# Kernel tuning notes

Hardware: AMD Instinct MI355X
Metric: run time of the kernel (lower is better)

The kernel has to match this reference:

```python
import jax, jax.numpy as jnp
from jax import lax
import numpy as np

B, T, D, H, LAT, FUT = 2048, 64, 64, 256, 64, 96
NL = 10  # LSTM layers


def _lstm_layer(x, Wih, Whh, b):
    # x: [B, T, Din]; Wih: [4H, Din]; Whh: [4H, H]; b: [4H]
    xg = jnp.einsum('btd,gd->tbg', x, Wih) + b  # precompute input projections [T,B,4H]
    h0 = jnp.zeros((x.shape[0], Whh.shape[1]), x.dtype)

    def step(carry, xt):
        h, c = carry
        g = xt + h @ Whh.T
        i, f, gg, o = jnp.split(g, 4, axis=-1)  # torch gate order i,f,g,o
        c = jax.nn.sigmoid(f) * c + jax.nn.sigmoid(i) * jnp.tanh(gg)
        h = jax.nn.sigmoid(o) * jnp.tanh(c)
        return (h, c), h

    _, hs = lax.scan(step, (h0, h0), xg)
    return jnp.transpose(hs, (1, 0, 2))  # [B,T,H]


def setup_inputs() -> dict:
    key = jax.random.key(0)
    ks = iter(jax.random.split(key, 40))
    s = 0.05
    n = lambda shape: jax.random.normal(next(ks), shape, jnp.float32) * s
    inp = {
        'X': jax.random.normal(next(ks), (B, T, D), jnp.float32),
        'Wih0': n((4 * H, D)),
        'Wih': n((NL - 1, 4 * H, H)),
        'Whh': n((NL, 4 * H, H)),
        'b': n((NL, 4 * H)),  # b_ih + b_hh folded together
        'ef1w': n((128, H)), 'ef1b': n((128,)),
        'ef2w': n((64, 128)), 'ef2b': n((64,)),
        'mean_w': n((LAT, 64)), 'mean_b': n((LAT,)),
        'logvar_w': n((LAT, 64)), 'logvar_b': n((LAT,)),
        'scale_w': n((LAT, 64)), 'scale_b': n((LAT,)),
        'shape_w': n((LAT, 64)), 'shape_b': n((LAT,)),
        'df1w': n((128, LAT)), 'df1b': n((128,)),
        'df2w': n((500, 128)), 'df2b': n((500,)),
        'outw': n((FUT, 500)), 'outb': n((FUT,)),
        'finw': n((FUT, FUT)), 'finb': n((FUT,)),
        'pi_gaussian': jnp.asarray(0.9, jnp.float32),
        'eps': jax.random.normal(next(ks), (B, LAT), jnp.float32),
        'u': jax.random.uniform(next(ks), (B, LAT), jnp.float32),
        'choice': jax.random.uniform(next(ks), (B,), jnp.float32),
    }
    return inp


def reference(X, Wih0, Wih, Whh, b, ef1w, ef1b, ef2w, ef2b,
              mean_w, mean_b, logvar_w, logvar_b, scale_w, scale_b,
              shape_w, shape_b, df1w, df1b, df2w, df2b, outw, outb,
              finw, finb, pi_gaussian, eps, u, choice):
    # ---- Encoder: 10-layer LSTM, last hidden state ----
    h = _lstm_layer(X, Wih0, Whh[0], b[0])
    for l in range(1, NL):
        h = _lstm_layer(h, Wih[l - 1], Whh[l], b[l])
    last = h[:, -1, :]  # [B,H]
    hid = jax.nn.relu(last @ ef1w.T + ef1b)
    hid = jax.nn.relu(hid @ ef2w.T + ef2b)  # dropout = identity (eval)
    z_mean = hid @ mean_w.T + mean_b
    z_logvar = hid @ logvar_w.T + logvar_b
    z_scale = jnp.exp(hid @ scale_w.T + scale_b)
    z_shape = hid @ shape_w.T + shape_b
    # ---- Reparameterize: vectorized gaussian/GPD row selection ----
    z_gauss = z_mean + eps * jnp.exp(0.5 * z_logvar)
    z_gpd = z_scale / z_shape * (jnp.exp(-z_shape * jnp.log1p(-u)) - 1.0)
    z = jnp.where(choice[:, None] < pi_gaussian, z_gauss, z_gpd)
    # ---- Decoder ----
    d = jax.nn.relu(z @ df1w.T + df1b)
    d = jax.nn.relu(d @ df2w.T + df2b)
    out = d @ outw.T + outb
    final = out @ finw.T + finb
    return (final, z_mean, z_logvar, z_scale, z_shape)
```

## Files before the change

### kernel.cpp

```cpp
#include <hip/hip_runtime.h>

typedef unsigned short u16;
typedef unsigned int   u32;
typedef _Float16 v8hf __attribute__((ext_vector_type(8)));
typedef float  f32x4 __attribute__((ext_vector_type(4)));

static constexpr int B_   = 2048;
static constexpr int T_   = 64;
static constexpr int D_   = 64;
static constexpr int H_   = 256;
static constexpr int NL_  = 10;
static constexpr int FUT_ = 96;
static constexpr int NBLK = 128;

static constexpr size_t WFH_OFF  = 0;
static constexpr size_t WFX_OFF  = 5u << 20;
static constexpr size_t XG_OFF   = 10u << 20;
static constexpr size_t SEQ2_OFF = 26u << 20;
static constexpr int    WFL9 = 262144;
static constexpr int    TCH  = 4;

__device__ __forceinline__ u16 f2h(float f) {
  _Float16 h = (_Float16)f;
  return __builtin_bit_cast(u16, h);
}
__device__ __forceinline__ float h2f(u16 b) {
  return (float)__builtin_bit_cast(_Float16, b);
}
__device__ __forceinline__ float rcp_(float x) { return __builtin_amdgcn_rcpf(x); }
__device__ __forceinline__ float fsig(float x) { return rcp_(1.f + __expf(-x)); }
__device__ __forceinline__ float ftanh(float x) {
  float e = __expf(-2.f * fabsf(x));
  float t = (1.f - e) * rcp_(1.f + e);
  return copysignf(t, x);
}
__device__ __forceinline__ void gld16(const u16* g, u16* l) {
  __builtin_amdgcn_global_load_lds(
      (const __attribute__((address_space(1))) void*)g,
      (__attribute__((address_space(3))) void*)l,
      16, 0, 0);
}

__global__ void pack_weights_v13(const float* __restrict__ Wih0,
                                 const float* __restrict__ Wih,
                                 const float* __restrict__ Whh,
                                 u16* __restrict__ wfh,
                                 u16* __restrict__ wfx) {
  int gid = blockIdx.x * 256 + threadIdx.x;
  int lw  = gid >> 15;
  if (lw >= NL_ * 2) return;
  int l = lw >> 1, which = lw & 1;
  int rem  = gid & 32767;
  int kc   = rem >> 12;
  int cg   = (rem >> 8) & 15;
  int g    = (rem >> 6) & 3;
  int lane = rem & 63;
  if (which == 1 && l == 0 && kc >= 2) return;

  int row = g * 256 + cg * 16 + (lane & 15);
  int k0  = kc * 32 + (lane >> 4) * 8;

  float v[8];
#pragma unroll
  for (int i = 0; i < 8; ++i) {
    int k = k0 + i;
    float x;
    if (which == 0)      x = Whh[(size_t)(l * 1024 + row) * 256 + k];
    else if (l == 0)     x = Wih0[row * 64 + k];
    else                 x = Wih[(size_t)((l - 1) * 1024 + row) * 256 + k];
    v[i] = x;
  }
  u32 pk[4];
#pragma unroll
  for (int i = 0; i < 4; ++i)
    pk[i] = (u32)f2h(v[2 * i]) | ((u32)f2h(v[2 * i + 1]) << 16);
  uint4 val; val.x = pk[0]; val.y = pk[1]; val.z = pk[2]; val.w = pk[3];
  u16* base = (which == 0) ? wfh : wfx;
  u16* dst = base + (size_t)l * WFL9
                  + ((size_t)(kc * 16 + cg) * 4 + g) * 512 + (size_t)lane * 8;
  *(uint4*)dst = val;
}

template <bool L0>
__global__ __launch_bounds__(1024, 4) void lstm_layer_v13(
    const float* __restrict__ X,
    u16* __restrict__ seq,
    const u16* __restrict__ wfx_l,
    const u16* __restrict__ wfh_l,
    u16* __restrict__ xg,
    const float* __restrict__ bias) {
  __shared__ __align__(16) u16 Wring[65536];
  __shared__ __align__(16) u16 Ah[16 * 256];

  const int tid  = threadIdx.x;
  const int wid  = tid >> 6;
  const int lane = tid & 63;
  const int bid  = blockIdx.x;
  const int arow = lane & 15;
  const int ahi  = lane >> 4;
  const int j    = wid * 16 + arow;

  *(uint2*)((char*)Ah + tid * 8) = make_uint2(0, 0);

  float c[4] = {0.f, 0.f, 0.f, 0.f};
  float bv[4];
#pragma unroll
  for (int g = 0; g < 4; ++g) bv[g] = bias[g * 256 + j];

  u16* slot0 = Wring + wid * 2048;
  u16* slot1 = Wring + 32768 + wid * 2048;
  const size_t laneoff = (size_t)lane * 8;
  u16* xgb = xg + (size_t)bid * 65536;
  uint2 xr[4];

  v8hf whr[4][4];
#pragma unroll
  for (int kc = 0; kc < 4; ++kc)
#pragma unroll
    for (int g = 0; g < 4; ++g)
      whr[kc][g] = *(const v8hf*)(const void*)(
          wfh_l + ((size_t)(kc * 16 + wid) * 4 + g) * 512 + laneoff);

  __syncthreads();

  for (int tc = 0; tc < T_ / TCH; ++tc) {
    f32x4 acc0[TCH][4];
#pragma unroll
    for (int rf = 0; rf < TCH; ++rf)
#pragma unroll
      for (int g = 0; g < 4; ++g) {
        acc0[rf][g][0] = bv[g]; acc0[rf][g][1] = bv[g];
        acc0[rf][g][2] = bv[g]; acc0[rf][g][3] = bv[g];
      }

    if constexpr (L0) {
#pragma unroll
      for (int g = 0; g < 4; ++g) {
        gld16(wfx_l + ((size_t)(0 * 16 + wid) * 4 + g) * 512 + laneoff, slot0 + g * 512);
        gld16(wfx_l + ((size_t)(1 * 16 + wid) * 4 + g) * 512 + laneoff, slot1 + g * 512);
      }
      asm volatile("s_waitcnt vmcnt(0)" ::: "memory");
      __builtin_amdgcn_sched_barrier(0);
      const float* xb = X + ((size_t)(bid * 16 + arow) * T_ + tc * TCH) * D_ + ahi * 8;
#pragma unroll
      for (int kc = 0; kc < 2; ++kc) {
        const u16* wl = (kc ? slot1 : slot0) + lane * 8;
        v8hf af[TCH];
#pragma unroll
        for (int rf = 0; rf < TCH; ++rf) {
          float4 u = *(const float4*)(xb + rf * D_ + kc * 32);
          float4 v2 = *(const float4*)(xb + rf * D_ + kc * 32 + 4);
          v8hf a;
          a[0] = (_Float16)u.x;  a[1] = (_Float16)u.y;
          a[2] = (_Float16)u.z;  a[3] = (_Float16)u.w;
          a[4] = (_Float16)v2.x; a[5] = (_Float16)v2.y;
          a[6] = (_Float16)v2.z; a[7] = (_Float16)v2.w;
          af[rf] = a;
        }
#pragma unroll
        for (int g = 0; g < 4; ++g) {
          v8hf w = *(const v8hf*)(const void*)(wl + g * 512);
#pragma unroll
          for (int rf = 0; rf < TCH; ++rf)
            acc0[rf][g] = __builtin_amdgcn_mfma_f32_16x16x32_f16(af[rf], w, acc0[rf][g], 0, 0, 0);
        }
      }
    } else {
      const u16* abase = seq + ((size_t)(bid * T_ + tc * TCH) * 16 + arow) * 256 + ahi * 8;
      v8hf aA[TCH], aB[TCH];
#pragma unroll
      for (int g = 0; g < 4; ++g)
        gld16(wfx_l + ((size_t)(0 * 16 + wid) * 4 + g) * 512 + laneoff, slot0 + g * 512);
#pragma unroll
      for (int rf = 0; rf < TCH; ++rf)
        aA[rf] = *(const v8hf*)(const void*)(abase + rf * 4096);

#pragma unroll
      for (int kc = 0; kc < 8; ++kc) {
        if (kc < 7) {
          u16* nd = ((kc + 1) & 1) ? slot1 : slot0;
#pragma unroll
          for (int g = 0; g < 4; ++g)
            gld16(wfx_l + ((size_t)((kc + 1) * 16 + wid) * 4 + g) * 512 + laneoff, nd + g * 512);
          if ((kc & 1) == 0) {
#pragma unroll
            for (int rf = 0; rf < TCH; ++rf)
              aB[rf] = *(const v8hf*)(const void*)(abase + rf * 4096 + (kc + 1) * 32);
          } else {
#pragma unroll
            for (int rf = 0; rf < TCH; ++rf)
              aA[rf] = *(const v8hf*)(const void*)(abase + rf * 4096 + (kc + 1) * 32);
          }
          asm volatile("s_waitcnt vmcnt(8)" ::: "memory");
        } else {
          asm volatile("s_waitcnt vmcnt(0)" ::: "memory");
        }
        __builtin_amdgcn_sched_barrier(0);
        const u16* wl = ((kc & 1) ? slot1 : slot0) + lane * 8;
#pragma unroll
        for (int g = 0; g < 4; ++g) {
          v8hf w = *(const v8hf*)(const void*)(wl + g * 512);
#pragma unroll
          for (int rf = 0; rf < TCH; ++rf)
            acc0[rf][g] = __builtin_amdgcn_mfma_f32_16x16x32_f16(
                ((kc & 1) ? aB[rf] : aA[rf]), w, acc0[rf][g], 0, 0, 0);
        }
      }
    }

#pragma unroll
    for (int rf = 0; rf < TCH; ++rf)
#pragma unroll
      for (int g = 0; g < 4; ++g) {
        uint2 pk;
        pk.x = (u32)f2h(acc0[rf][g][0]) | ((u32)f2h(acc0[rf][g][1]) << 16);
        pk.y = (u32)f2h(acc0[rf][g][2]) | ((u32)f2h(acc0[rf][g][3]) << 16);
        *(uint2*)(xgb + (((size_t)(rf * 1024 + g * 256 + j)) << 4) + ahi * 4) = pk;
      }
    __syncthreads();

#pragma unroll
    for (int g = 0; g < 4; ++g)
      xr[g] = *(const uint2*)(xgb + (((size_t)(0 * 1024 + g * 256 + j)) << 4) + ahi * 4);

    for (int tl = 0; tl < TCH; ++tl) {
      const int t = tc * TCH + tl;
      f32x4 acc[4];
#pragma unroll
      for (int g = 0; g < 4; ++g) {
        acc[g][0] = h2f((u16)(xr[g].x & 0xffff));
        acc[g][1] = h2f((u16)(xr[g].x >> 16));
        acc[g][2] = h2f((u16)(xr[g].y & 0xffff));
        acc[g][3] = h2f((u16)(xr[g].y >> 16));
      }

#pragma unroll
      for (int g = 0; g < 4; ++g)
        gld16(wfh_l + ((size_t)(4 * 16 + wid) * 4 + g) * 512 + laneoff, slot0 + g * 512);
#pragma unroll
      for (int g = 0; g < 4; ++g)
        gld16(wfh_l + ((size_t)(5 * 16 + wid) * 4 + g) * 512 + laneoff, slot1 + g * 512);

#pragma unroll
      for (int kc = 0; kc < 4; ++kc) {
        v8hf a = *(const v8hf*)((const char*)Ah + arow * 512 +
                                ((kc * 64 + ahi * 16) ^ ((arow & 7) << 4)));
#pragma unroll
        for (int g = 0; g < 4; ++g)
          acc[g] = __builtin_amdgcn_mfma_f32_16x16x32_f16(a, whr[kc][g], acc[g], 0, 0, 0);
      }

      asm volatile("s_waitcnt vmcnt(4)" ::: "memory");
      __builtin_amdgcn_sched_barrier(0);
      {
        v8hf a = *(const v8hf*)((const char*)Ah + arow * 512 +
                                ((4 * 64 + ahi * 16) ^ ((arow & 7) << 4)));
        const u16* wl = slot0 + lane * 8;
#pragma unroll
        for (int g = 0; g < 4; ++g) {
          v8hf w = *(const v8hf*)(const void*)(wl + g * 512);
          acc[g] = __builtin_amdgcn_mfma_f32_16x16x32_f16(a, w, acc[g], 0, 0, 0);
        }
      }
#pragma unroll
      for (int g = 0; g < 4; ++g)
        gld16(wfh_l + ((size_t)(6 * 16 + wid) * 4 + g) * 512 + laneoff, slot0 + g * 512);
      asm volatile("s_waitcnt vmcnt(4)" ::: "memory");
      __builtin_amdgcn_sched_barrier(0);
      {
        v8hf a = *(const v8hf*)((const char*)Ah + arow * 512 +
                                ((5 * 64 + ahi * 16) ^ ((arow & 7) << 4)));
        const u16* wl = slot1 + lane * 8;
#pragma unroll
        for (int g = 0; g < 4; ++g) {
          v8hf w = *(const v8hf*)(const void*)(wl + g * 512);
          acc[g] = __builtin_amdgcn_mfma_f32_16x16x32_f16(a, w, acc[g], 0, 0, 0);
        }
      }
#pragma unroll
      for (int g = 0; g < 4; ++g)
        gld16(wfh_l + ((size_t)(7 * 16 + wid) * 4 + g) * 512 + laneoff, slot1 + g * 512);
      asm volatile("s_waitcnt vmcnt(4)" ::: "memory");
      __builtin_amdgcn_sched_barrier(0);
      {
        v8hf a = *(const v8hf*)((const char*)Ah + arow * 512 +
                                ((6 * 64 + ahi * 16) ^ ((arow & 7) << 4)));
        const u16* wl = slot0 + lane * 8;
#pragma unroll
        for (int g = 0; g < 4; ++g) {
          v8hf w = *(const v8hf*)(const void*)(wl + g * 512);
          acc[g] = __builtin_amdgcn_mfma_f32_16x16x32_f16(a, w, acc[g], 0, 0, 0);
        }
      }
      asm volatile("s_waitcnt vmcnt(0)" ::: "memory");
      __builtin_amdgcn_sched_barrier(0);
      {
        v8hf a = *(const v8hf*)((const char*)Ah + arow * 512 +
                                ((7 * 64 + ahi * 16) ^ ((arow & 7) << 4)));
        const u16* wl = slot1 + lane * 8;
#pragma unroll
        for (int g = 0; g < 4; ++g) {
          v8hf w = *(const v8hf*)(const void*)(wl + g * 512);
          acc[g] = __builtin_amdgcn_mfma_f32_16x16x32_f16(a, w, acc[g], 0, 0, 0);
        }
      }
      __syncthreads();

      if (tl + 1 < TCH) {
#pragma unroll
        for (int g = 0; g < 4; ++g)
          xr[g] = *(const uint2*)(xgb + (((size_t)((tl + 1) * 1024 + g * 256 + j)) << 4) + ahi * 4);
      }

      u16* sbase = seq + ((((size_t)bid * T_ + t) * 16) << 8) + j;
#pragma unroll
      for (int q = 0; q < 4; ++q) {
        int r = ahi * 4 + q;
        float cn = fsig(acc[1][q]) * c[q] + fsig(acc[0][q]) * ftanh(acc[2][q]);
        c[q] = cn;
        float h = fsig(acc[3][q]) * ftanh(cn);
        u16 hb = f2h(h);
        sbase[(size_t)r << 8] = hb;
        *(u16*)((char*)Ah + r * 512 + ((j * 2) ^ ((r & 7) << 4))) = hb;
      }
      __syncthreads();
    }
  }
}

template <int N, int K, bool RELU>
__device__ __forceinline__ void dense(const float (*__restrict__ in)[512],
                                      float (*__restrict__ out)[512],
                                      const float* __restrict__ W,
                                      const float* __restrict__ bg, int tid) {
  for (int e = tid; e < 16 * N; e += 256) {
    int r = e / N, n = e - r * N;
    const float* wr = W + (size_t)n * K;
    const float* ar = in[r];
    float4 acc = {0.f, 0.f, 0.f, 0.f};
    for (int k = 0; k < K; k += 4) {
      float4 wv = *(const float4*)(wr + k);
      float4 av = *(const float4*)(ar + k);
      acc.x = fmaf(wv.x, av.x, acc.x);
      acc.y = fmaf(wv.y, av.y, acc.y);
      acc.z = fmaf(wv.z, av.z, acc.z);
      acc.w = fmaf(wv.w, av.w, acc.w);
    }
    float s = bg[n] + acc.x + acc.y + acc.z + acc.w;
    out[r][n] = RELU ? fmaxf(s, 0.f) : s;
  }
}

template <int K>
__device__ __forceinline__ float dotK(const float* __restrict__ a, const float* __restrict__ w) {
  float4 acc = {0.f, 0.f, 0.f, 0.f};
#pragma unroll
  for (int k = 0; k < K; k += 4) {
    float4 wv = *(const float4*)(w + k);
    float4 av = *(const float4*)(a + k);
    acc.x = fmaf(wv.x, av.x, acc.x);
    acc.y = fmaf(wv.y, av.y, acc.y);
    acc.z = fmaf(wv.z, av.z, acc.z);
    acc.w = fmaf(wv.w, av.w, acc.w);
  }
  return acc.x + acc.y + acc.z + acc.w;
}

struct TailArgs {
  const u16* seq;
  const float *ef1w, *ef1b, *ef2w, *ef2b;
  const float *mean_w, *mean_b, *logvar_w, *logvar_b;
  const float *scale_w, *scale_b, *shape_w, *shape_b;
  const float *df1w, *df1b, *df2w, *df2b, *outw, *outb, *finw, *finb;
  const float *pi, *eps, *u, *choice;
  float* out;
};

__global__ __launch_bounds__(256) void tail_kernel_v13(TailArgs A) {
  __shared__ float a0[16][512];
  __shared__ float a1[16][512];
  const int tid = threadIdx.x, bid = blockIdx.x;

  for (int e = tid; e < 16 * 256; e += 256) {
    int r = e >> 8, jj = e & 255;
    a0[r][jj] = h2f(A.seq[((((size_t)bid * T_ + (T_ - 1)) * 16 + r) << 8) + jj]);
  }
  __syncthreads();

  dense<128, 256, true>(a0, a1, A.ef1w, A.ef1b, tid); __syncthreads();
  dense<64, 128, true>(a1, a0, A.ef2w, A.ef2b, tid);  __syncthreads();

  const float pi = *A.pi;
  for (int e = tid; e < 16 * 64; e += 256) {
    int r = e >> 6, n = e & 63;
    size_t rg = (size_t)bid * 16 + r;
    float m  = dotK<64>(a0[r], A.mean_w   + n * 64) + A.mean_b[n];
    float lv = dotK<64>(a0[r], A.logvar_w + n * 64) + A.logvar_b[n];
    float sc = __expf(dotK<64>(a0[r], A.scale_w + n * 64) + A.scale_b[n]);
    float sh = dotK<64>(a0[r], A.shape_w + n * 64) + A.shape_b[n];
    A.out[196608 + rg * 64 + n] = m;
    A.out[327680 + rg * 64 + n] = lv;
    A.out[458752 + rg * 64 + n] = sc;
    A.out[589824 + rg * 64 + n] = sh;
    float zg = m + A.eps[rg * 64 + n] * __expf(0.5f * lv);
    float L  = log1pf(-A.u[rg * 64 + n]);
    float zp = sc / sh * (__expf(-sh * L) - 1.f);
    a1[r][n] = (A.choice[rg] < pi) ? zg : zp;
  }
  __syncthreads();

  dense<128, 64, true>(a1, a0, A.df1w, A.df1b, tid);   __syncthreads();
  dense<500, 128, true>(a0, a1, A.df2w, A.df2b, tid);  __syncthreads();
  dense<96, 500, false>(a1, a0, A.outw, A.outb, tid);  __syncthreads();
  dense<96, 96, false>(a0, a1, A.finw, A.finb, tid);   __syncthreads();

  for (int e = tid; e < 16 * FUT_; e += 256) {
    int r = e / FUT_, n = e - r * FUT_;
    A.out[((size_t)bid * 16 + r) * FUT_ + n] = a1[r][n];
  }
}

extern "C" void kernel_launch(void* const* d_in, const int* in_sizes, int n_in,
                              void* d_out, int out_size, void* d_ws, size_t ws_size,
                              hipStream_t stream) {
  (void)in_sizes; (void)n_in; (void)out_size; (void)ws_size;

  const float* X      = (const float*)d_in[0];
  const float* Wih0   = (const float*)d_in[1];
  const float* Wih    = (const float*)d_in[2];
  const float* Whh    = (const float*)d_in[3];
  const float* b      = (const float*)d_in[4];
  const float* ef1w   = (const float*)d_in[5];
  const float* ef1b   = (const float*)d_in[6];
  const float* ef2w   = (const float*)d_in[7];
  const float* ef2b   = (const float*)d_in[8];
  const float* mean_w = (const float*)d_in[9];
  const float* mean_b = (const float*)d_in[10];
  const float* logvar_w = (const float*)d_in[11];
  const float* logvar_b = (const float*)d_in[12];
  const float* scale_w  = (const float*)d_in[13];
  const float* scale_b  = (const float*)d_in[14];
  const float* shape_w  = (const float*)d_in[15];
  const float* shape_b  = (const float*)d_in[16];
  const float* df1w   = (const float*)d_in[17];
  const float* df1b   = (const float*)d_in[18];
  const float* df2w   = (const float*)d_in[19];
  const float* df2b   = (const float*)d_in[20];
  const float* outw   = (const float*)d_in[21];
  const float* outb   = (const float*)d_in[22];
  const float* finw   = (const float*)d_in[23];
  const float* finb   = (const float*)d_in[24];
  const float* pi_g   = (const float*)d_in[25];
  const float* eps    = (const float*)d_in[26];
  const float* u      = (const float*)d_in[27];
  const float* choice = (const float*)d_in[28];

  float* out = (float*)d_out;
  u16* wfh = (u16*)((char*)d_ws + WFH_OFF);
  u16* wfx = (u16*)((char*)d_ws + WFX_OFF);
  u16* xg  = (u16*)((char*)d_ws + XG_OFF);
  u16* seq = (u16*)((char*)d_ws + SEQ2_OFF);

  pack_weights_v13<<<2560, 256, 0, stream>>>(Wih0, Wih, Whh, wfh, wfx);

  lstm_layer_v13<true><<<NBLK, 1024, 0, stream>>>(X, seq, wfx, wfh, xg, b);
  for (int l = 1; l < NL_; ++l)
    lstm_layer_v13<false><<<NBLK, 1024, 0, stream>>>(nullptr, seq,
        wfx + (size_t)l * WFL9, wfh + (size_t)l * WFL9, xg, b + l * 1024);

  TailArgs A;
  A.seq = seq;
  A.ef1w = ef1w; A.ef1b = ef1b; A.ef2w = ef2w; A.ef2b = ef2b;
  A.mean_w = mean_w; A.mean_b = mean_b; A.logvar_w = logvar_w; A.logvar_b = logvar_b;
  A.scale_w = scale_w; A.scale_b = scale_b; A.shape_w = shape_w; A.shape_b = shape_b;
  A.df1w = df1w; A.df1b = df1b; A.df2w = df2w; A.df2b = df2b;
  A.outw = outw; A.outb = outb; A.finw = finw; A.finb = finb;
  A.pi = pi_g; A.eps = eps; A.u = u; A.choice = choice;
  A.out = out;
  tail_kernel_v13<<<NBLK, 256, 0, stream>>>(A);
}
```

Before: 11.93 ms.

## Keep input-gate projections in registers and stream all recurrent weights through LDS

The input projections for each time chunk are now packed to fp16 and kept in registers (xr[TCH][4]). Before, they were written to a global xg scratch buffer and read back. This removes the global round trip and a block-wide barrier. The recurrent weight chunks 0-3 that used to live in registers (whr) are now streamed through the LDS double-buffer ring like chunks 4-7, with an 8-step pipelined loop. That frees registers but adds global-to-LDS weight traffic every time step, which raises load latency on the serial recurrence path.

Measured after the change: 11.09 ms. 1.08x faster.

```diff
diff --git a/kernel.cpp b/kernel.cpp
--- a/kernel.cpp
+++ b/kernel.cpp
@@ -15,7 +15,6 @@
 
 static constexpr size_t WFH_OFF  = 0;
 static constexpr size_t WFX_OFF  = 5u << 20;
-static constexpr size_t XG_OFF   = 10u << 20;
 static constexpr size_t SEQ2_OFF = 26u << 20;
 static constexpr int    WFL9 = 262144;
 static constexpr int    TCH  = 4;
@@ -41,7 +40,7 @@
       16, 0, 0);
 }
 
-__global__ void pack_weights_v13(const float* __restrict__ Wih0,
+__global__ void pack_weights_v14(const float* __restrict__ Wih0,
                                  const float* __restrict__ Wih,
                                  const float* __restrict__ Whh,
                                  u16* __restrict__ wfh,
@@ -82,12 +81,11 @@
 }
 
 template <bool L0>
-__global__ __launch_bounds__(1024, 4) void lstm_layer_v13(
+__global__ __launch_bounds__(1024, 4) void lstm_layer_v14(
     const float* __restrict__ X,
     u16* __restrict__ seq,
     const u16* __restrict__ wfx_l,
     const u16* __restrict__ wfh_l,
-    u16* __restrict__ xg,
     const float* __restrict__ bias) {
   __shared__ __align__(16) u16 Wring[65536];
   __shared__ __align__(16) u16 Ah[16 * 256];
@@ -110,16 +108,6 @@
   u16* slot0 = Wring + wid * 2048;
   u16* slot1 = Wring + 32768 + wid * 2048;
   const size_t laneoff = (size_t)lane * 8;
-  u16* xgb = xg + (size_t)bid * 65536;
-  uint2 xr[4];
-
-  v8hf whr[4][4];
-#pragma unroll
-  for (int kc = 0; kc < 4; ++kc)
-#pragma unroll
-    for (int g = 0; g < 4; ++g)
-      whr[kc][g] = *(const v8hf*)(const void*)(
-          wfh_l + ((size_t)(kc * 16 + wid) * 4 + g) * 512 + laneoff);
 
   __syncthreads();
 
@@ -209,99 +197,53 @@
     }
 
 #pragma unroll
+    for (int g = 0; g < 4; ++g)
+      gld16(wfh_l + ((size_t)(0 * 16 + wid) * 4 + g) * 512 + laneoff, slot0 + g * 512);
+#pragma unroll
+    for (int g = 0; g < 4; ++g)
+      gld16(wfh_l + ((size_t)(1 * 16 + wid) * 4 + g) * 512 + laneoff, slot1 + g * 512);
+
+    uint2 xr[TCH][4];
+#pragma unroll
     for (int rf = 0; rf < TCH; ++rf)
 #pragma unroll
       for (int g = 0; g < 4; ++g) {
-        uint2 pk;
-        pk.x = (u32)f2h(acc0[rf][g][0]) | ((u32)f2h(acc0[rf][g][1]) << 16);
-        pk.y = (u32)f2h(acc0[rf][g][2]) | ((u32)f2h(acc0[rf][g][3]) << 16);
-        *(uint2*)(xgb + (((size_t)(rf * 1024 + g * 256 + j)) << 4) + ahi * 4) = pk;
-      }
-    __syncthreads();
-
-#pragma unroll
-    for (int g = 0; g < 4; ++g)
-      xr[g] = *(const uint2*)(xgb + (((size_t)(0 * 1024 + g * 256 + j)) << 4) + ahi * 4);
-
+        xr[rf][g].x = (u32)f2h(acc0[rf][g][0]) | ((u32)f2h(acc0[rf][g][1]) << 16);
+        xr[rf][g].y = (u32)f2h(acc0[rf][g][2]) | ((u32)f2h(acc0[rf][g][3]) << 16);
+      }
+
+#pragma unroll
     for (int tl = 0; tl < TCH; ++tl) {
       const int t = tc * TCH + tl;
       f32x4 acc[4];
 #pragma unroll
       for (int g = 0; g < 4; ++g) {
-        acc[g][0] = h2f((u16)(xr[g].x & 0xffff));
-        acc[g][1] = h2f((u16)(xr[g].x >> 16));
-        acc[g][2] = h2f((u16)(xr[g].y & 0xffff));
-        acc[g][3] = h2f((u16)(xr[g].y >> 16));
-      }
-
-#pragma unroll
-      for (int g = 0; g < 4; ++g)
-        gld16(wfh_l + ((size_t)(4 * 16 + wid) * 4 + g) * 512 + laneoff, slot0 + g * 512);
-#pragma unroll
-      for (int g = 0; g < 4; ++g)
-        gld16(wfh_l + ((size_t)(5 * 16 + wid) * 4 + g) * 512 + laneoff, slot1 + g * 512);
-
-#pragma unroll
-      for (int kc = 0; kc < 4; ++kc) {
+        acc[g][0] = h2f((u16)(xr[tl][g].x & 0xffff));
+        acc[g][1] = h2f((u16)(xr[tl][g].x >> 16));
+        acc[g][2] = h2f((u16)(xr[tl][g].y & 0xffff));
+        acc[g][3] = h2f((u16)(xr[tl][g].y >> 16));
+      }
+
+#pragma unroll
+      for (int kc = 0; kc < 8; ++kc) {
+        if (kc < 7) asm volatile("s_waitcnt vmcnt(4)" ::: "memory");
+        else        asm volatile("s_waitcnt vmcnt(0)" ::: "memory");
+        __builtin_amdgcn_sched_barrier(0);
+
         v8hf a = *(const v8hf*)((const char*)Ah + arow * 512 +
                                 ((kc * 64 + ahi * 16) ^ ((arow & 7) << 4)));
-#pragma unroll
-        for (int g = 0; g < 4; ++g)
-          acc[g] = __builtin_amdgcn_mfma_f32_16x16x32_f16(a, whr[kc][g], acc[g], 0, 0, 0);
-      }
-
-      asm volatile("s_waitcnt vmcnt(4)" ::: "memory");
-      __builtin_amdgcn_sched_barrier(0);
-      {
-        v8hf a = *(const v8hf*)((const char*)Ah + arow * 512 +
-                                ((4 * 64 + ahi * 16) ^ ((arow & 7) << 4)));
-        const u16* wl = slot0 + lane * 8;
+        const u16* wl = ((kc & 1) ? slot1 : slot0) + lane * 8;
 #pragma unroll
         for (int g = 0; g < 4; ++g) {
           v8hf w = *(const v8hf*)(const void*)(wl + g * 512);
           acc[g] = __builtin_amdgcn_mfma_f32_16x16x32_f16(a, w, acc[g], 0, 0, 0);
         }
-      }
-#pragma unroll
-      for (int g = 0; g < 4; ++g)
-        gld16(wfh_l + ((size_t)(6 * 16 + wid) * 4 + g) * 512 + laneoff, slot0 + g * 512);
-      asm volatile("s_waitcnt vmcnt(4)" ::: "memory");
-      __builtin_amdgcn_sched_barrier(0);
-      {
-        v8hf a = *(const v8hf*)((const char*)Ah + arow * 512 +
-                                ((5 * 64 + ahi * 16) ^ ((arow & 7) << 4)));
-        const u16* wl = slot1 + lane * 8;
-#pragma unroll
-        for (int g = 0; g < 4; ++g) {
-          v8hf w = *(const v8hf*)(const void*)(wl + g * 512);
-          acc[g] = __builtin_amdgcn_mfma_f32_16x16x32_f16(a, w, acc[g], 0, 0, 0);
-        }
-      }
-#pragma unroll
-      for (int g = 0; g < 4; ++g)
-        gld16(wfh_l + ((size_t)(7 * 16 + wid) * 4 + g) * 512 + laneoff, slot1 + g * 512);
-      asm volatile("s_waitcnt vmcnt(4)" ::: "memory");
-      __builtin_amdgcn_sched_barrier(0);
-      {
-        v8hf a = *(const v8hf*)((const char*)Ah + arow * 512 +
-                                ((6 * 64 + ahi * 16) ^ ((arow & 7) << 4)));
-        const u16* wl = slot0 + lane * 8;
-#pragma unroll
-        for (int g = 0; g < 4; ++g) {
-          v8hf w = *(const v8hf*)(const void*)(wl + g * 512);
-          acc[g] = __builtin_amdgcn_mfma_f32_16x16x32_f16(a, w, acc[g], 0, 0, 0);
-        }
-      }
-      asm volatile("s_waitcnt vmcnt(0)" ::: "memory");
-      __builtin_amdgcn_sched_barrier(0);
-      {
-        v8hf a = *(const v8hf*)((const char*)Ah + arow * 512 +
-                                ((7 * 64 + ahi * 16) ^ ((arow & 7) << 4)));
-        const u16* wl = slot1 + lane * 8;
-#pragma unroll
-        for (int g = 0; g < 4; ++g) {
-          v8hf w = *(const v8hf*)(const void*)(wl + g * 512);
-          acc[g] = __builtin_amdgcn_mfma_f32_16x16x32_f16(a, w, acc[g], 0, 0, 0);
+        if (kc < 6) {
+          u16* nd = (kc & 1) ? slot1 : slot0;
+#pragma unroll
+          for (int g = 0; g < 4; ++g)
+            gld16(wfh_l + ((size_t)((kc + 2) * 16 + wid) * 4 + g) * 512 + laneoff,
+                  nd + g * 512);
         }
       }
       __syncthreads();
@@ -309,7 +251,10 @@
       if (tl + 1 < TCH) {
 #pragma unroll
         for (int g = 0; g < 4; ++g)
-          xr[g] = *(const uint2*)(xgb + (((size_t)((tl + 1) * 1024 + g * 256 + j)) << 4) + ahi * 4);
+          gld16(wfh_l + ((size_t)(0 * 16 + wid) * 4 + g) * 512 + laneoff, slot0 + g * 512);
+#pragma unroll
+        for (int g = 0; g < 4; ++g)
+          gld16(wfh_l + ((size_t)(1 * 16 + wid) * 4 + g) * 512 + laneoff, slot1 + g * 512);
       }
 
       u16* sbase = seq + ((((size_t)bid * T_ + t) * 16) << 8) + j;
@@ -376,7 +321,7 @@
   float* out;
 };
 
-__global__ __launch_bounds__(256) void tail_kernel_v13(TailArgs A) {
+__global__ __launch_bounds__(256) void tail_kernel_v14(TailArgs A) {
   __shared__ float a0[16][512];
   __shared__ float a1[16][512];
   const int tid = threadIdx.x, bid = blockIdx.x;
@@ -458,15 +403,14 @@
   float* out = (float*)d_out;
   u16* wfh = (u16*)((char*)d_ws + WFH_OFF);
   u16* wfx = (u16*)((char*)d_ws + WFX_OFF);
-  u16* xg  = (u16*)((char*)d_ws + XG_OFF);
   u16* seq = (u16*)((char*)d_ws + SEQ2_OFF);
 
-  pack_weights_v13<<<2560, 256, 0, stream>>>(Wih0, Wih, Whh, wfh, wfx);
-
-  lstm_layer_v13<true><<<NBLK, 1024, 0, stream>>>(X, seq, wfx, wfh, xg, b);
+  pack_weights_v14<<<2560, 256, 0, stream>>>(Wih0, Wih, Whh, wfh, wfx);
+
+  lstm_layer_v14<true><<<NBLK, 1024, 0, stream>>>(X, seq, wfx, wfh, b);
   for (int l = 1; l < NL_; ++l)
-    lstm_layer_v13<false><<<NBLK, 1024, 0, stream>>>(nullptr, seq,
-        wfx + (size_t)l * WFL9, wfh + (size_t)l * WFL9, xg, b + l * 1024);
+    lstm_layer_v14<false><<<NBLK, 1024, 0, stream>>>(nullptr, seq,
+        wfx + (size_t)l * WFL9, wfh + (size_t)l * WFL9, b + l * 1024);
 
   TailArgs A;
   A.seq = seq;
@@ -477,5 +421,5 @@
   A.outw = outw; A.outb = outb; A.finw = finw; A.finb = finb;
   A.pi = pi_g; A.eps = eps; A.u = u; A.choice = choice;
   A.out = out;
-  tail_kernel_v13<<<NBLK, 256, 0, stream>>>(A);
-}
+  tail_kernel_v14<<<NBLK, 256, 0, stream>>>(A);
+}
```
